# Optimization experiments

Hardware: AMD Instinct MI355X
Metric: run time of the kernel (lower is better)

The kernel has to match this reference:

```python
import jax, jax.numpy as jnp
import numpy as np

N_NODES = 100000
N_EDGES = 1600000
D_IN = 128
D_OUT = 128


def setup_inputs() -> dict:
    key = jax.random.key(0)
    k1, k2, k3, k4, k5 = jax.random.split(key, 5)
    x = jax.random.normal(k1, (N_NODES, D_IN), dtype=jnp.float32)
    # nn.Linear weight has shape [out_features, in_features]
    W = jax.random.normal(k2, (D_OUT, D_IN), dtype=jnp.float32) * (1.0 / np.sqrt(D_IN))
    adj_rows = jax.random.randint(k3, (N_EDGES,), 0, N_NODES, dtype=jnp.int32)
    adj_cols = jax.random.randint(k4, (N_EDGES,), 0, N_NODES, dtype=jnp.int32)
    adj_vals = jax.random.uniform(k5, (N_EDGES,), dtype=jnp.float32)
    return {"x": x, "W": W, "adj_rows": adj_rows, "adj_cols": adj_cols, "adj_vals": adj_vals}


def reference(x, W, adj_rows, adj_cols, adj_vals):
    # x: [N, D_in] node features; W: [D_out, D_in] linear weight (bias=False)
    h = jnp.einsum('ni,oi->no', x, W)  # dense projection, [N, D_out]
    # sparse adjacency matmul: out[r] = sum_e vals[e] * h[cols[e]] for rows[e]==r
    messages = adj_vals[:, None] * h[adj_cols]  # [E, D_out]
    out = jax.ops.segment_sum(messages, adj_rows, num_segments=x.shape[0])
    return out
```

## Files before the change

kernel.cpp:

```cpp
#include <hip/hip_runtime.h>

#define D 128
#define RPB 512
#define RPB_SHIFT 9
#define HALF 256
#define BUCKMAX 256
#define TILE 8192
#define SEGCAP 7168

typedef short bf16x8 __attribute__((ext_vector_type(8)));
typedef float f32x4 __attribute__((ext_vector_type(4)));

__device__ inline unsigned short f2bf(float f) {
    unsigned u = __float_as_uint(f);
    unsigned r = u + 0x7FFFu + ((u >> 16) & 1u);
    return (unsigned short)(r >> 16);
}

__global__ __launch_bounds__(256) void cast_x(const float* __restrict__ src,
                                              unsigned short* __restrict__ dst,
                                              long long n4,
                                              int* __restrict__ bucketCnt) {
    if (blockIdx.x == 0) bucketCnt[threadIdx.x & (BUCKMAX - 1)] = 0;
    long long i = (long long)blockIdx.x * 256 + threadIdx.x;
    const long long stride = (long long)gridDim.x * 256;
    for (; i < n4; i += stride) {
        float4 v = reinterpret_cast<const float4*>(src)[i];
        ushort4 o;
        o.x = f2bf(v.x); o.y = f2bf(v.y); o.z = f2bf(v.z); o.w = f2bf(v.w);
        reinterpret_cast<ushort4*>(dst)[i] = o;
    }
}

__global__ __launch_bounds__(1024) void bucket_hist(const int* __restrict__ rows,
                                                    int* __restrict__ bucketCnt,
                                                    int E, int NBUCK) {
    __shared__ int h[BUCKMAX];
    for (int i = threadIdx.x; i < NBUCK; i += 1024) h[i] = 0;
    __syncthreads();
    const int t0 = blockIdx.x * TILE;
    const int tend = min(t0 + TILE, E);
    for (int i = t0 + threadIdx.x; i < tend; i += 1024)
        atomicAdd(&h[rows[i] >> RPB_SHIFT], 1);
    __syncthreads();
    for (int i = threadIdx.x; i < NBUCK; i += 1024)
        if (h[i]) atomicAdd(&bucketCnt[i], h[i]);
}

__global__ __launch_bounds__(256) void scan_castW(const int* __restrict__ bucketCnt,
                                                  int* __restrict__ bucketBase,
                                                  int* __restrict__ bucketCur,
                                                  int* __restrict__ offsets,
                                                  int NBUCK, int N,
                                                  const float* __restrict__ W,
                                                  unsigned short* __restrict__ Wb) {
    const int tid = threadIdx.x;
    if (blockIdx.x == 1) {
        for (int idx = tid; idx < D * D / 4; idx += 256) {
            float4 v = reinterpret_cast<const float4*>(W)[idx];
            ushort4 o;
            o.x = f2bf(v.x); o.y = f2bf(v.y); o.z = f2bf(v.z); o.w = f2bf(v.w);
            reinterpret_cast<ushort4*>(Wb)[idx] = o;
        }
        return;
    }
    __shared__ int t[256];
    int v = (tid < NBUCK) ? bucketCnt[tid] : 0;
    t[tid] = v;
    __syncthreads();
    for (int ofs = 1; ofs < 256; ofs <<= 1) {
        int add = (tid >= ofs) ? t[tid - ofs] : 0;
        __syncthreads();
        t[tid] += add;
        __syncthreads();
    }
    if (tid < NBUCK) {
        bucketBase[tid] = t[tid] - v;
        bucketCur[tid] = 0;
    }
    if (tid == NBUCK - 1) {
        bucketBase[NBUCK] = t[tid];
        offsets[N] = t[tid];
    }
}

__global__ __launch_bounds__(1024) void binA(const int* __restrict__ rows,
                                             const int* __restrict__ cols,
                                             const float* __restrict__ vals,
                                             const int* __restrict__ bucketBase,
                                             int* __restrict__ bucketCur,
                                             uint2* __restrict__ pairs_bin,
                                             int E, int NBUCK) {
    __shared__ int h[BUCKMAX];
    __shared__ int base[BUCKMAX];
    const int t0 = blockIdx.x * TILE;
    const int tend = min(t0 + TILE, E);
    for (int i = threadIdx.x; i < NBUCK; i += 1024) h[i] = 0;
    __syncthreads();

    int rreg[8];
#pragma unroll
    for (int k = 0; k < 8; ++k) {
        const int i = t0 + threadIdx.x + k * 1024;
        rreg[k] = (i < tend) ? rows[i] : -1;
        if (rreg[k] >= 0) atomicAdd(&h[rreg[k] >> RPB_SHIFT], 1);
    }
    __syncthreads();
    for (int i = threadIdx.x; i < NBUCK; i += 1024) {
        int c = h[i];
        base[i] = c ? bucketBase[i] + atomicAdd(&bucketCur[i], c) : 0;
        h[i] = 0;
    }
    __syncthreads();
#pragma unroll
    for (int k = 0; k < 8; ++k) {
        const int i = t0 + threadIdx.x + k * 1024;
        if (i < tend) {
            const int r = rreg[k];
            const int b = r >> RPB_SHIFT;
            const int p = base[b] + atomicAdd(&h[b], 1);
            const unsigned pk = ((unsigned)(r & (RPB - 1)) << 23) | (unsigned)cols[i];
            pairs_bin[p] = make_uint2(pk, __float_as_uint(vals[i]));
        }
    }
}

__global__ __launch_bounds__(256) void csr_build(const uint2* __restrict__ pairs_bin,
                                                 const int* __restrict__ bucketBase,
                                                 int* __restrict__ offsets,
                                                 uint2* __restrict__ pairs_g, int N) {
    __shared__ int hist[HALF];
    __shared__ int cur[HALF];
    __shared__ int tsum[256];
    __shared__ uint2 pr[SEGCAP];
    __shared__ int cntBelowSh;
    const int tid = threadIdx.x;
    const int buck = blockIdx.x >> 1, half = blockIdx.x & 1;
    const int lrow0 = half * HALF;
    const int grow0 = buck * RPB + lrow0;
    const int rbeg = bucketBase[buck], rend = bucketBase[buck + 1];

    hist[tid] = 0;
    if (tid == 0) cntBelowSh = 0;
    __syncthreads();

    int below = 0;
    for (int i = rbeg + tid; i < rend; i += 256) {
        int d = (int)(pairs_bin[i].x >> 23) - lrow0;
        if ((unsigned)d < (unsigned)HALF) atomicAdd(&hist[d], 1);
        else if (d < 0) ++below;
    }
    if (below) atomicAdd(&cntBelowSh, below);
    __syncthreads();

    int part = hist[tid];
    tsum[tid] = part;
    __syncthreads();
    for (int ofs = 1; ofs < 256; ofs <<= 1) {
        int add = (tid >= ofs) ? tsum[tid - ofs] : 0;
        __syncthreads();
        tsum[tid] += add;
        __syncthreads();
    }
    const int excl = tsum[tid] - part;
    const int segcnt = tsum[255];
    const int segbase = rbeg + cntBelowSh;

    cur[tid] = excl;
    const int grow = grow0 + tid;
    if (grow < N) offsets[grow] = segbase + excl;
    __syncthreads();

    if (segcnt <= SEGCAP) {
        for (int i = rbeg + tid; i < rend; i += 256) {
            uint2 e = pairs_bin[i];
            int d = (int)(e.x >> 23) - lrow0;
            if ((unsigned)d < (unsigned)HALF) {
                int p = atomicAdd(&cur[d], 1);
                pr[p] = make_uint2(e.x & 0x7FFFFFu, e.y);
            }
        }
        __syncthreads();
        for (int p = tid; p < segcnt; p += 256) pairs_g[segbase + p] = pr[p];
    } else {
        for (int i = rbeg + tid; i < rend; i += 256) {
            uint2 e = pairs_bin[i];
            int d = (int)(e.x >> 23) - lrow0;
            if ((unsigned)d < (unsigned)HALF) {
                int p = atomicAdd(&cur[d], 1);
                pairs_g[segbase + p] = make_uint2(e.x & 0x7FFFFFu, e.y);
            }
        }
    }
}

__global__ __launch_bounds__(256) void csr_gather_bf16(
    const unsigned short* __restrict__ xb,
    const int* __restrict__ offsets,
    const uint2* __restrict__ pairs,
    unsigned short* __restrict__ yb, int N) {
    __shared__ uint2 prl[4][64];
    const int row = blockIdx.x * 4 + (threadIdx.x >> 6);
    if (row >= N) return;
    const int wave = threadIdx.x >> 6;
    const int lane = threadIdx.x & 63;
    const int g    = lane >> 4;
    const int c8   = lane & 15;
    const int beg = offsets[row], end = offsets[row + 1];

    float a[8] = {};
    for (int base = beg; base < end; base += 64) {
        const int rem = min(end - base, 64);
        uint2 e = make_uint2(0u, 0u);
        if (lane < rem) e = pairs[base + lane];
        prl[wave][lane] = e;
        __builtin_amdgcn_wave_barrier();

        for (int j0 = 0; j0 < rem; j0 += 16) {
            uint2 pe[4];
            uint4 u[4];
#pragma unroll
            for (int i = 0; i < 4; ++i)
                pe[i] = prl[wave][j0 + 4 * i + g];
#pragma unroll
            for (int i = 0; i < 4; ++i)
                u[i] = *reinterpret_cast<const uint4*>(
                    xb + (size_t)pe[i].x * D + c8 * 8);
#pragma unroll
            for (int i = 0; i < 4; ++i) {
                const float v = __uint_as_float(pe[i].y);
                const unsigned w0 = u[i].x, w1 = u[i].y, w2 = u[i].z, w3 = u[i].w;
                a[0] = fmaf(v, __uint_as_float(w0 << 16), a[0]);
                a[1] = fmaf(v, __uint_as_float(w0 & 0xFFFF0000u), a[1]);
                a[2] = fmaf(v, __uint_as_float(w1 << 16), a[2]);
                a[3] = fmaf(v, __uint_as_float(w1 & 0xFFFF0000u), a[3]);
                a[4] = fmaf(v, __uint_as_float(w2 << 16), a[4]);
                a[5] = fmaf(v, __uint_as_float(w2 & 0xFFFF0000u), a[5]);
                a[6] = fmaf(v, __uint_as_float(w3 << 16), a[6]);
                a[7] = fmaf(v, __uint_as_float(w3 & 0xFFFF0000u), a[7]);
            }
        }
        __builtin_amdgcn_wave_barrier();
    }

#pragma unroll
    for (int i = 0; i < 8; ++i) {
        a[i] += __shfl_xor(a[i], 16);
        a[i] += __shfl_xor(a[i], 32);
    }
    if (g == 0) {
        uint4 o;
        o.x = (unsigned)f2bf(a[0]) | ((unsigned)f2bf(a[1]) << 16);
        o.y = (unsigned)f2bf(a[2]) | ((unsigned)f2bf(a[3]) << 16);
        o.z = (unsigned)f2bf(a[4]) | ((unsigned)f2bf(a[5]) << 16);
        o.w = (unsigned)f2bf(a[6]) | ((unsigned)f2bf(a[7]) << 16);
        *reinterpret_cast<uint4*>(yb + (size_t)row * D + c8 * 8) = o;
    }
}

__global__ __launch_bounds__(256) void gemm_mfma(const unsigned short* __restrict__ yb,
                                                 const unsigned short* __restrict__ Wb,
                                                 float* __restrict__ out, int N) {
    const int wid  = threadIdx.x >> 6;
    const int lane = threadIdx.x & 63;
    const int m0   = blockIdx.x * 64 + wid * 16;
    const int r    = lane & 15;
    const int kg   = lane >> 4;
    const int arow = m0 + r;

    f32x4 acc[8] = {};
#pragma unroll
    for (int ks = 0; ks < 4; ++ks) {
        const int k0 = ks * 32 + kg * 8;
        bf16x8 a = {};
        if (arow < N) a = *reinterpret_cast<const bf16x8*>(yb + (size_t)arow * D + k0);
#pragma unroll
        for (int t = 0; t < 8; ++t) {
            bf16x8 b = *reinterpret_cast<const bf16x8*>(Wb + (size_t)(t * 16 + r) * D + k0);
            acc[t] = __builtin_amdgcn_mfma_f32_16x16x32_bf16(a, b, acc[t], 0, 0, 0);
        }
    }
#pragma unroll
    for (int t = 0; t < 8; ++t) {
#pragma unroll
        for (int i = 0; i < 4; ++i) {
            const int row = m0 + kg * 4 + i;
            if (row < N) out[(size_t)row * D + t * 16 + r] = acc[t][i];
        }
    }
}

__global__ __launch_bounds__(256) void gemm64(const float* __restrict__ x,
                                              const float* __restrict__ W,
                                              float* __restrict__ h, int N) {
    __shared__ float xs[128][64];
    __shared__ float ws[128][64];
    const int tid = threadIdx.x;
    const int m0 = blockIdx.x * 64;
    const int n0 = blockIdx.y * 64;
    for (int idx = tid; idx < 2048; idx += 256) {
        int q = idx >> 6, m = idx & 63;
        int grow = m0 + m;
        float4 v = make_float4(0.f, 0.f, 0.f, 0.f);
        if (grow < N) v = *reinterpret_cast<const float4*>(x + (size_t)grow * D + q * 4);
        xs[q * 4 + 0][m] = v.x; xs[q * 4 + 1][m] = v.y;
        xs[q * 4 + 2][m] = v.z; xs[q * 4 + 3][m] = v.w;
    }
    for (int idx = tid; idx < 2048; idx += 256) {
        int q = idx >> 6, n = idx & 63;
        float4 v = *reinterpret_cast<const float4*>(W + (size_t)(n0 + n) * D + q * 4);
        ws[q * 4 + 0][n] = v.x; ws[q * 4 + 1][n] = v.y;
        ws[q * 4 + 2][n] = v.z; ws[q * 4 + 3][n] = v.w;
    }
    __syncthreads();
    const int tm = (tid & 15) * 4;
    const int tn = (tid >> 4) * 4;
    float acc[4][4] = {};
#pragma unroll 4
    for (int k = 0; k < 128; ++k) {
        float4 a4 = *reinterpret_cast<const float4*>(&xs[k][tm]);
        float4 b4 = *reinterpret_cast<const float4*>(&ws[k][tn]);
        float a[4] = {a4.x, a4.y, a4.z, a4.w};
        float b[4] = {b4.x, b4.y, b4.z, b4.w};
#pragma unroll
        for (int rr = 0; rr < 4; ++rr)
#pragma unroll
            for (int cc = 0; cc < 4; ++cc) acc[rr][cc] = fmaf(a[rr], b[cc], acc[rr][cc]);
    }
#pragma unroll
    for (int rr = 0; rr < 4; ++rr) {
        int row = m0 + tm + rr;
        if (row < N) {
            float4 o = make_float4(acc[rr][0], acc[rr][1], acc[rr][2], acc[rr][3]);
            *reinterpret_cast<float4*>(h + (size_t)row * D + n0 + tn) = o;
        }
    }
}

__global__ __launch_bounds__(256) void scatter_edges(const float* __restrict__ h,
                                                     const int* __restrict__ rows,
                                                     const int* __restrict__ cols,
                                                     const float* __restrict__ vals,
                                                     float* __restrict__ out, int E) {
    int t = blockIdx.x * 256 + threadIdx.x;
    int e = t >> 5;
    if (e >= E) return;
    int q = t & 31;
    int r = rows[e];
    int c = cols[e];
    float v = vals[e];
    float4 m = reinterpret_cast<const float4*>(h + (size_t)c * D)[q];
    float* op = out + (size_t)r * D + q * 4;
    atomicAdd(op + 0, v * m.x);
    atomicAdd(op + 1, v * m.y);
    atomicAdd(op + 2, v * m.z);
    atomicAdd(op + 3, v * m.w);
}

extern "C" void kernel_launch(void* const* d_in, const int* in_sizes, int n_in,
                              void* d_out, int out_size, void* d_ws, size_t ws_size,
                              hipStream_t stream) {
    const float* x        = (const float*)d_in[0];
    const float* W        = (const float*)d_in[1];
    const int*   adj_rows = (const int*)d_in[2];
    const int*   adj_cols = (const int*)d_in[3];
    const float* adj_vals = (const float*)d_in[4];
    float* out = (float*)d_out;

    const int N = in_sizes[0] / D;
    const int E = in_sizes[2];
    const int NBUCK = (N + RPB - 1) / RPB;
    const int NT = (E + TILE - 1) / TILE;

    size_t off = 0;
    auto carve = [&](size_t bytes) {
        void* p = (char*)d_ws + off;
        off += (bytes + 255) & ~(size_t)255;
        return p;
    };
    unsigned short* xb = (unsigned short*)carve((size_t)N * D * 2);
    unsigned short* yb = (unsigned short*)carve((size_t)N * D * 2);
    unsigned short* Wb = (unsigned short*)carve((size_t)D * D * 2);
    int* offsets    = (int*)carve((size_t)(N + 1) * sizeof(int));
    int* bucketCnt  = (int*)carve((size_t)BUCKMAX * sizeof(int));
    int* bucketBase = (int*)carve((size_t)(BUCKMAX + 1) * sizeof(int));
    int* bucketCur  = (int*)carve((size_t)BUCKMAX * sizeof(int));
    const size_t wsNeed = off;

    size_t doff = 0;
    auto carveOut = [&](size_t bytes) {
        void* p = (char*)d_out + doff;
        doff += (bytes + 255) & ~(size_t)255;
        return p;
    };
    uint2* pairs_bin = (uint2*)carveOut((size_t)E * sizeof(uint2));
    uint2* pairs_g   = (uint2*)carveOut((size_t)E * sizeof(uint2));
    const size_t doutNeed = doff;

    const bool fits = (wsNeed <= ws_size) &&
                      (doutNeed <= (size_t)out_size * sizeof(float)) &&
                      (NBUCK <= BUCKMAX) && (N < (1 << 23));

    if (fits) {
        cast_x<<<2048, 256, 0, stream>>>(x, xb, (long long)N * (D / 4), bucketCnt);
        bucket_hist<<<NT, 1024, 0, stream>>>(adj_rows, bucketCnt, E, NBUCK);
        scan_castW<<<2, 256, 0, stream>>>(bucketCnt, bucketBase, bucketCur,
                                          offsets, NBUCK, N, W, Wb);
        binA<<<NT, 1024, 0, stream>>>(adj_rows, adj_cols, adj_vals, bucketBase,
                                      bucketCur, pairs_bin, E, NBUCK);
        csr_build<<<NBUCK * 2, 256, 0, stream>>>(pairs_bin, bucketBase,
                                                 offsets, pairs_g, N);
        csr_gather_bf16<<<(N + 3) / 4, 256, 0, stream>>>(xb, offsets, pairs_g, yb, N);
        gemm_mfma<<<(N + 63) / 64, 256, 0, stream>>>(yb, Wb, out, N);
    } else {
        float* h = (float*)d_ws;
        hipMemsetAsync(d_out, 0, (size_t)out_size * sizeof(float), stream);
        dim3 ggrid((N + 63) / 64, D / 64);
        gemm64<<<ggrid, 256, 0, stream>>>(x, W, h, N);
        const long long tt = (long long)E * 32;
        scatter_edges<<<(int)((tt + 255) / 256), 256, 0, stream>>>(
            h, adj_rows, adj_cols, adj_vals, out, E);
    }
}
```

Baseline: 158.6 us.

## Fuse bucket histogram into cast kernel and shrink buckets to 256 rows

Merges the x-to-bf16 cast with the row-bucket histogram into one kernel, removing a launch. Halves rows per bucket so there are twice as many buckets, and csr_build now runs one block per bucket over all of its rows. This drops the old half-bucket split, which made each block read the whole bucket and filter out half of it. The scan is widened to handle up to 512 buckets with two entries per thread. The cost is more buckets contending in binA's atomics, plus a dependency of the histogram pass on the cast loop inside the same kernel.

New measurement: 178.7 us. 1.13x slower.

```diff
diff --git a/kernel.cpp b/kernel.cpp
--- a/kernel.cpp
+++ b/kernel.cpp
@@ -1,10 +1,9 @@
 #include <hip/hip_runtime.h>
 
 #define D 128
-#define RPB 512
-#define RPB_SHIFT 9
-#define HALF 256
-#define BUCKMAX 256
+#define RPB 256
+#define RPB_SHIFT 8
+#define BUCKMAX 512
 #define TILE 8192
 #define SEGCAP 7168
 
@@ -17,33 +16,36 @@
     return (unsigned short)(r >> 16);
 }
 
-__global__ __launch_bounds__(256) void cast_x(const float* __restrict__ src,
-                                              unsigned short* __restrict__ dst,
-                                              long long n4,
-                                              int* __restrict__ bucketCnt) {
-    if (blockIdx.x == 0) bucketCnt[threadIdx.x & (BUCKMAX - 1)] = 0;
-    long long i = (long long)blockIdx.x * 256 + threadIdx.x;
-    const long long stride = (long long)gridDim.x * 256;
-    for (; i < n4; i += stride) {
-        float4 v = reinterpret_cast<const float4*>(src)[i];
-        ushort4 o;
-        o.x = f2bf(v.x); o.y = f2bf(v.y); o.z = f2bf(v.z); o.w = f2bf(v.w);
-        reinterpret_cast<ushort4*>(dst)[i] = o;
-    }
-}
-
-__global__ __launch_bounds__(1024) void bucket_hist(const int* __restrict__ rows,
-                                                    int* __restrict__ bucketCnt,
-                                                    int E, int NBUCK) {
+__global__ __launch_bounds__(256) void cast_x_hist(const float* __restrict__ x,
+                                                   unsigned short* __restrict__ xb,
+                                                   long long n4,
+                                                   const int* __restrict__ rows,
+                                                   int* __restrict__ bucketCnt,
+                                                   int E, int NBUCK) {
+    if (blockIdx.x == 0) {
+        bucketCnt[threadIdx.x] = 0;
+        bucketCnt[threadIdx.x + 256] = 0;
+    }
+    {
+        long long i = (long long)blockIdx.x * 256 + threadIdx.x;
+        const long long stride = (long long)gridDim.x * 256;
+        for (; i < n4; i += stride) {
+            float4 v = reinterpret_cast<const float4*>(x)[i];
+            ushort4 o;
+            o.x = f2bf(v.x); o.y = f2bf(v.y); o.z = f2bf(v.z); o.w = f2bf(v.w);
+            reinterpret_cast<ushort4*>(xb)[i] = o;
+        }
+    }
     __shared__ int h[BUCKMAX];
-    for (int i = threadIdx.x; i < NBUCK; i += 1024) h[i] = 0;
-    __syncthreads();
-    const int t0 = blockIdx.x * TILE;
-    const int tend = min(t0 + TILE, E);
-    for (int i = t0 + threadIdx.x; i < tend; i += 1024)
-        atomicAdd(&h[rows[i] >> RPB_SHIFT], 1);
-    __syncthreads();
-    for (int i = threadIdx.x; i < NBUCK; i += 1024)
+    for (int i = threadIdx.x; i < BUCKMAX; i += 256) h[i] = 0;
+    __syncthreads();
+    {
+        long long i = (long long)blockIdx.x * 256 + threadIdx.x;
+        const long long stride = (long long)gridDim.x * 256;
+        for (; i < E; i += stride) atomicAdd(&h[rows[i] >> RPB_SHIFT], 1);
+    }
+    __syncthreads();
+    for (int i = threadIdx.x; i < NBUCK; i += 256)
         if (h[i]) atomicAdd(&bucketCnt[i], h[i]);
 }
 
@@ -65,8 +67,11 @@
         return;
     }
     __shared__ int t[256];
-    int v = (tid < NBUCK) ? bucketCnt[tid] : 0;
-    t[tid] = v;
+    const int i0 = tid * 2, i1 = tid * 2 + 1;
+    int v0 = (i0 < NBUCK) ? bucketCnt[i0] : 0;
+    int v1 = (i1 < NBUCK) ? bucketCnt[i1] : 0;
+    int s = v0 + v1;
+    t[tid] = s;
     __syncthreads();
     for (int ofs = 1; ofs < 256; ofs <<= 1) {
         int add = (tid >= ofs) ? t[tid - ofs] : 0;
@@ -74,13 +79,12 @@
         t[tid] += add;
         __syncthreads();
     }
-    if (tid < NBUCK) {
-        bucketBase[tid] = t[tid] - v;
-        bucketCur[tid] = 0;
-    }
-    if (tid == NBUCK - 1) {
-        bucketBase[NBUCK] = t[tid];
-        offsets[N] = t[tid];
+    const int base0 = t[tid] - s;
+    if (i0 < NBUCK) { bucketBase[i0] = base0;      bucketCur[i0] = 0; }
+    if (i1 < NBUCK) { bucketBase[i1] = base0 + v0; bucketCur[i1] = 0; }
+    if (tid == 255) {
+        bucketBase[NBUCK] = t[255];
+        offsets[N] = t[255];
     }
 }
 
@@ -95,7 +99,7 @@
     __shared__ int base[BUCKMAX];
     const int t0 = blockIdx.x * TILE;
     const int tend = min(t0 + TILE, E);
-    for (int i = threadIdx.x; i < NBUCK; i += 1024) h[i] = 0;
+    for (int i = threadIdx.x; i < BUCKMAX; i += 1024) h[i] = 0;
     __syncthreads();
 
     int rreg[8];
@@ -129,28 +133,20 @@
                                                  const int* __restrict__ bucketBase,
                                                  int* __restrict__ offsets,
                                                  uint2* __restrict__ pairs_g, int N) {
-    __shared__ int hist[HALF];
-    __shared__ int cur[HALF];
+    __shared__ int hist[RPB];
+    __shared__ int cur[RPB];
     __shared__ int tsum[256];
     __shared__ uint2 pr[SEGCAP];
-    __shared__ int cntBelowSh;
     const int tid = threadIdx.x;
-    const int buck = blockIdx.x >> 1, half = blockIdx.x & 1;
-    const int lrow0 = half * HALF;
-    const int grow0 = buck * RPB + lrow0;
+    const int buck = blockIdx.x;
+    const int grow0 = buck * RPB;
     const int rbeg = bucketBase[buck], rend = bucketBase[buck + 1];
 
     hist[tid] = 0;
-    if (tid == 0) cntBelowSh = 0;
-    __syncthreads();
-
-    int below = 0;
-    for (int i = rbeg + tid; i < rend; i += 256) {
-        int d = (int)(pairs_bin[i].x >> 23) - lrow0;
-        if ((unsigned)d < (unsigned)HALF) atomicAdd(&hist[d], 1);
-        else if (d < 0) ++below;
-    }
-    if (below) atomicAdd(&cntBelowSh, below);
+    __syncthreads();
+
+    for (int i = rbeg + tid; i < rend; i += 256)
+        atomicAdd(&hist[pairs_bin[i].x >> 23], 1);
     __syncthreads();
 
     int part = hist[tid];
@@ -164,32 +160,25 @@
     }
     const int excl = tsum[tid] - part;
     const int segcnt = tsum[255];
-    const int segbase = rbeg + cntBelowSh;
 
     cur[tid] = excl;
     const int grow = grow0 + tid;
-    if (grow < N) offsets[grow] = segbase + excl;
+    if (grow < N) offsets[grow] = rbeg + excl;
     __syncthreads();
 
     if (segcnt <= SEGCAP) {
         for (int i = rbeg + tid; i < rend; i += 256) {
             uint2 e = pairs_bin[i];
-            int d = (int)(e.x >> 23) - lrow0;
-            if ((unsigned)d < (unsigned)HALF) {
-                int p = atomicAdd(&cur[d], 1);
-                pr[p] = make_uint2(e.x & 0x7FFFFFu, e.y);
-            }
+            int p = atomicAdd(&cur[e.x >> 23], 1);
+            pr[p] = make_uint2(e.x & 0x7FFFFFu, e.y);
         }
         __syncthreads();
-        for (int p = tid; p < segcnt; p += 256) pairs_g[segbase + p] = pr[p];
+        for (int p = tid; p < segcnt; p += 256) pairs_g[rbeg + p] = pr[p];
     } else {
         for (int i = rbeg + tid; i < rend; i += 256) {
             uint2 e = pairs_bin[i];
-            int d = (int)(e.x >> 23) - lrow0;
-            if ((unsigned)d < (unsigned)HALF) {
-                int p = atomicAdd(&cur[d], 1);
-                pairs_g[segbase + p] = make_uint2(e.x & 0x7FFFFFu, e.y);
-            }
+            int p = atomicAdd(&cur[e.x >> 23], 1);
+            pairs_g[rbeg + p] = make_uint2(e.x & 0x7FFFFFu, e.y);
         }
     }
 }
@@ -402,14 +391,14 @@
                       (NBUCK <= BUCKMAX) && (N < (1 << 23));
 
     if (fits) {
-        cast_x<<<2048, 256, 0, stream>>>(x, xb, (long long)N * (D / 4), bucketCnt);
-        bucket_hist<<<NT, 1024, 0, stream>>>(adj_rows, bucketCnt, E, NBUCK);
+        cast_x_hist<<<2048, 256, 0, stream>>>(x, xb, (long long)N * (D / 4),
+                                              adj_rows, bucketCnt, E, NBUCK);
         scan_castW<<<2, 256, 0, stream>>>(bucketCnt, bucketBase, bucketCur,
                                           offsets, NBUCK, N, W, Wb);
         binA<<<NT, 1024, 0, stream>>>(adj_rows, adj_cols, adj_vals, bucketBase,
                                       bucketCur, pairs_bin, E, NBUCK);
-        csr_build<<<NBUCK * 2, 256, 0, stream>>>(pairs_bin, bucketBase,
-                                                 offsets, pairs_g, N);
+        csr_build<<<NBUCK, 256, 0, stream>>>(pairs_bin, bucketBase,
+                                             offsets, pairs_g, N);
         csr_gather_bf16<<<(N + 3) / 4, 256, 0, stream>>>(xb, offsets, pairs_g, yb, N);
         gemm_mfma<<<(N + 63) / 64, 256, 0, stream>>>(yb, Wb, out, N);
     } else {
```
